# Performance work log

Hardware: AMD Instinct MI355X
Metric: run time of the kernel (lower is better)

The kernel has to match this reference:

```python
import jax, jax.numpy as jnp
import numpy as np

K = 20  # neighbors
SLOPE = 0.2  # leaky relu negative slope


def knn_idx(x):
    # x: [B, C, N] -> idx: [B, N, K] indices of K nearest points (incl. self)
    inner = -2.0 * jnp.einsum('bcn,bcm->bnm', x, x)          # [B,N,N]
    xx = jnp.sum(x * x, axis=1)                              # [B,N]
    pairwise = -xx[:, :, None] - inner - xx[:, None, :]      # negative sq dist
    _, idx = jax.lax.top_k(pairwise, K)                      # [B,N,K]
    return idx


def graph_feature(x, idx):
    # x: [B, C, N], idx: [B, N, K] -> [B, N, K, 2C] = cat(neighbor - center, center)
    xt = jnp.transpose(x, (0, 2, 1))                         # [B,N,C]
    nbr = jnp.take_along_axis(xt[:, None, :, :], idx[..., None], axis=2)  # [B,N,K,C]
    ctr = jnp.broadcast_to(xt[:, :, None, :], nbr.shape)     # [B,N,K,C]
    return jnp.concatenate([nbr - ctr, ctr], axis=-1)        # [B,N,K,2C]


def edge_block(x, W):
    # x: [B, C, N]; W: [C_out, 2C] (1x1 conv weight, no bias)
    f = graph_feature(x, knn_idx(x))                         # [B,N,K,2C]
    y = jnp.einsum('bnkc,oc->bonk', f, W)                    # [B,C_out,N,K]
    y = jax.nn.leaky_relu(y, negative_slope=SLOPE)
    return jnp.max(y, axis=-1)                               # [B,C_out,N]


def setup_inputs() -> dict:
    key = jax.random.key(0)
    ks = jax.random.split(key, 6)
    B, N = 8, 2048
    x = jax.random.normal(ks[0], (B, 3, N), dtype=jnp.float32)
    def w(k, o, i):
        return jax.random.normal(k, (o, i), dtype=jnp.float32) * (1.0 / np.sqrt(i))
    W1 = w(ks[1], 64, 6)      # block1: in 3  -> 64
    W2 = w(ks[2], 64, 128)    # block2: in 64 -> 64
    W3 = w(ks[3], 128, 128)   # block3: in 64 -> 128
    W4 = w(ks[4], 256, 256)   # block4: in 128-> 256
    Wg = w(ks[5], 1024, 512)  # global conv1d: 64+64+128+256=512 -> 1024
    return {'x': x, 'W1': W1, 'W2': W2, 'W3': W3, 'W4': W4, 'Wg': Wg}


def reference(x, W1, W2, W3, W4, Wg):
    x1 = edge_block(x, W1)                                   # [B,64,N]
    x2 = edge_block(x1, W2)                                  # [B,64,N]
    x3 = edge_block(x2, W3)                                  # [B,128,N]
    x4 = edge_block(x3, W4)                                  # [B,256,N]
    x_cat = jnp.concatenate([x1, x2, x3, x4], axis=1)        # [B,512,N]
    g = jnp.einsum('bcn,oc->bon', x_cat, Wg)                 # [B,1024,N]
    g = jax.nn.leaky_relu(g, negative_slope=SLOPE)
    return jnp.max(g, axis=-1)                               # [B,1024]
```

## Files before the change

kernel.cpp:

```cpp
#include <hip/hip_runtime.h>
#include <hip/hip_bf16.h>
#include <cfloat>

#define Nn 2048
#define KK 20
#define BB 8
#define SLOPE 0.2f
#define NCH 32

typedef __bf16 bf16x8 __attribute__((ext_vector_type(8)));
typedef float f32x4 __attribute__((ext_vector_type(4)));
typedef unsigned short u16x8 __attribute__((ext_vector_type(8)));

__device__ __forceinline__ unsigned short bfbits(__hip_bfloat16 h) {
    unsigned short us;
    __builtin_memcpy(&us, &h, 2);
    return us;
}


__global__ void wfrag_all(const float* __restrict__ W1, const float* __restrict__ W2,
                          const float* __restrict__ W3, const float* __restrict__ W4,
                          __hip_bfloat16* __restrict__ base) {
    int g = blockIdx.x * 256 + threadIdx.x;
    const float* W; int CIN, Co, CO2, KS; long hoff; int go;
    if (g < 512)        { go = g;        CIN = 3;   Co = 64;  CO2 = 128; KS = 1; hoff = 0;     W = W1; }
    else if (g < 1536)  { go = g - 512;  CIN = 64;  Co = 64;  CO2 = 128; KS = 2; hoff = 8192;  W = W2; }
    else if (g < 3584)  { go = g - 1536; CIN = 64;  Co = 128; CO2 = 256; KS = 2; hoff = 24576; W = W3; }
    else if (g < 11776) { go = g - 3584; CIN = 128; Co = 256; CO2 = 512; KS = 4; hoff = 57344; W = W4; }
    else return;
    int o = go / (KS * 4);
    int c8 = (go - o * (KS * 4)) * 8;
    long lsz = (long)(CO2 / 16) * KS * 512;
    __hip_bfloat16* Wh = base + hoff;
    __hip_bfloat16* Wl = Wh + lsz;
    u16x8 hw, lw;
    #pragma unroll
    for (int t = 0; t < 8; ++t) {
        int c = c8 + t;
        float v = 0.f;
        if (c < CIN) {
            if (o < Co) v = W[(long)o * 2 * CIN + c];
            else        v = W[(long)(o - Co) * 2 * CIN + CIN + c] - W[(long)(o - Co) * 2 * CIN + c];
        }
        __hip_bfloat16 h = __float2bfloat16(v);
        hw[t] = bfbits(h);
        lw[t] = bfbits(__float2bfloat16(v - __bfloat162float(h)));
    }
    long dst = ((long)(o >> 4) * KS + (c8 >> 5)) * 512 + ((o & 15) + 16 * ((c8 >> 3) & 3)) * 8;
    *(u16x8*)(Wh + dst) = hw;
    *(u16x8*)(Wl + dst) = lw;
}

__global__ void tobf16_frag(const float* __restrict__ W, __hip_bfloat16* __restrict__ F) {
    int g = blockIdx.x * 256 + threadIdx.x;
    if (g >= 1024 * 64) return;
    int o = g >> 6, k8 = (g & 63) * 8;
    const float* src = W + (long)o * 512 + k8;
    unsigned short tmp[8];
    #pragma unroll
    for (int t = 0; t < 8; ++t) tmp[t] = bfbits(__float2bfloat16(src[t]));
    long dst = ((long)(o >> 4) * 16 + (k8 >> 5)) * 512 + ((o & 15) + 16 * ((k8 >> 3) & 3)) * 8;
    u16x8 pk;
    #pragma unroll
    for (int t = 0; t < 8; ++t) pk[t] = tmp[t];
    *(u16x8*)(F + dst) = pk;
}

__global__ void split3_kernel(const float* __restrict__ x,
                              __hip_bfloat16* __restrict__ xh,
                              __hip_bfloat16* __restrict__ xl,
                              float* __restrict__ sq) {
    int i = blockIdx.x * 256 + threadIdx.x;
    if (i >= BB * Nn) return;
    const float* xb = x + (long)(i >> 11) * 3 * Nn + (i & 2047);
    float v0 = xb[0], v1 = xb[Nn], v2 = xb[2 * Nn];
    sq[i] = v0 * v0 + v1 * v1 + v2 * v2;
    __hip_bfloat16 h0 = __float2bfloat16(v0), h1 = __float2bfloat16(v1), h2 = __float2bfloat16(v2);
    __hip_bfloat16 l0 = __float2bfloat16(v0 - __bfloat162float(h0));
    __hip_bfloat16 l1 = __float2bfloat16(v1 - __bfloat162float(h1));
    __hip_bfloat16 l2 = __float2bfloat16(v2 - __bfloat162float(h2));
    long base = ((long)(i >> 11) * 128 + ((i & 2047) >> 4)) * 512 + (long)(i & 15) * 8;
    u16x8 z = (u16x8){0, 0, 0, 0, 0, 0, 0, 0};
    u16x8 hw = z, lw = z;
    hw[0] = bfbits(h0); hw[1] = bfbits(h1); hw[2] = bfbits(h2);
    lw[0] = bfbits(l0); lw[1] = bfbits(l1); lw[2] = bfbits(l2);
    *(u16x8*)(xh + base) = hw;
    *(u16x8*)(xl + base) = lw;
    #pragma unroll
    for (int q = 1; q < 4; ++q) {
        *(u16x8*)(xh + base + q * 128) = z;
        *(u16x8*)(xl + base + q * 128) = z;
    }
}

__device__ __forceinline__ unsigned fkey(float f) {
    unsigned u = __float_as_uint(f);
    return u ^ (((unsigned)((int)u >> 31)) | 0x80000000u);
}

template<int C, int NKS>
__global__ void __launch_bounds__(512)
gram_mfma(const __hip_bfloat16* __restrict__ xh, const __hip_bfloat16* __restrict__ xl,
          int ks0, const float* __restrict__ sqv, unsigned* __restrict__ Kbuf) {
    constexpr int KS = C / 32;
    const int tid = threadIdx.x;
    const int w = tid >> 6, lane = tid & 63;
    const int lm = lane & 15, quad = lane >> 4;
    const int wg = (blockIdx.x & 7) * 128 + (blockIdx.x >> 3);
    const int nb = wg & 7;
    const int mt = (wg >> 3) & 15;
    const int b  = wg >> 7;
    const int m0 = mt * 128 + (w >> 2) * 64;
    const int j0 = nb * 256 + (w & 3) * 64;

    const long TILE = (long)NKS * 512;
    const __hip_bfloat16* hbase = xh + (long)b * 128 * TILE + (long)ks0 * 512 + lane * 8;
    const __hip_bfloat16* lbase = xl + (long)b * 128 * TILE + (long)ks0 * 512 + lane * 8;
    const __hip_bfloat16* hA = hbase + (long)(m0 >> 4) * TILE;
    const __hip_bfloat16* lA = lbase + (long)(m0 >> 4) * TILE;
    const __hip_bfloat16* hB = hbase + (long)(j0 >> 4) * TILE;
    const __hip_bfloat16* lB = lbase + (long)(j0 >> 4) * TILE;

    f32x4 acc[4][4];
    #pragma unroll
    for (int i = 0; i < 4; ++i)
        #pragma unroll
        for (int j = 0; j < 4; ++j)
            acc[i][j] = (f32x4){0.f, 0.f, 0.f, 0.f};

    #pragma unroll 2
    for (int ks = 0; ks < KS; ++ks) {
        bf16x8 ah[4], alo[4], bh[4], blo[4];
        #pragma unroll
        for (int i = 0; i < 4; ++i) {
            ah[i]  = *(const bf16x8*)(const void*)(hA + (long)i * TILE + ks * 512);
            alo[i] = *(const bf16x8*)(const void*)(lA + (long)i * TILE + ks * 512);
        }
        #pragma unroll
        for (int j = 0; j < 4; ++j) {
            bh[j]  = *(const bf16x8*)(const void*)(hB + (long)j * TILE + ks * 512);
            blo[j] = *(const bf16x8*)(const void*)(lB + (long)j * TILE + ks * 512);
        }
        #pragma unroll
        for (int i = 0; i < 4; ++i)
            #pragma unroll
            for (int j = 0; j < 4; ++j) {
                acc[i][j] = __builtin_amdgcn_mfma_f32_16x16x32_bf16(alo[i], bh[j], acc[i][j], 0, 0, 0);
                acc[i][j] = __builtin_amdgcn_mfma_f32_16x16x32_bf16(ah[i], blo[j], acc[i][j], 0, 0, 0);
                acc[i][j] = __builtin_amdgcn_mfma_f32_16x16x32_bf16(ah[i], bh[j], acc[i][j], 0, 0, 0);
            }
    }

    const float* sqb = sqv + b * Nn;
    float sqj[4];
    #pragma unroll
    for (int j = 0; j < 4; ++j) sqj[j] = sqb[j0 + j * 16 + lm];

    unsigned* Kb = Kbuf + (long)b * Nn * Nn;
    #pragma unroll
    for (int i = 0; i < 4; ++i) {
        #pragma unroll
        for (int r = 0; r < 4; ++r) {
            int m = m0 + i * 16 + quad * 4 + r;
            uint4 kv;
            kv.x = fkey(fmaf(-2.f, acc[i][0][r], sqj[0]));
            kv.y = fkey(fmaf(-2.f, acc[i][1][r], sqj[1]));
            kv.z = fkey(fmaf(-2.f, acc[i][2][r], sqj[2]));
            kv.w = fkey(fmaf(-2.f, acc[i][3][r], sqj[3]));
            *(uint4*)(Kb + (long)m * Nn + j0 + lm * 4) = kv;
        }
    }
}

template<int KS, int NKS_A, int CO2>
__global__ void __launch_bounds__(256)
proj_mfma(const __hip_bfloat16* __restrict__ Ah, const __hip_bfloat16* __restrict__ Al,
          int ks0,
          const __hip_bfloat16* __restrict__ Wh, const __hip_bfloat16* __restrict__ Wl,
          float* __restrict__ Z) {
    constexpr int NWo = (CO2 >= 256) ? 4 : 2;
    constexpr int NWm = 4 / NWo;
    constexpr int MT = 2048 / (64 * NWm);
    const int tid = threadIdx.x;
    const int w = tid >> 6, lane = tid & 63;
    const int lm = lane & 15, quad = lane >> 4;
    const int b  = blockIdx.x & 7;
    const int mt = (blockIdx.x >> 3) % MT;
    const int ot = (blockIdx.x >> 3) / MT;
    const int m0 = mt * 64 * NWm + (w / NWo) * 64;
    const int o0 = ot * 64 * NWo + (w % NWo) * 64;

    const long TA = (long)NKS_A * 512;
    const long TW = (long)KS * 512;
    const __hip_bfloat16* hA = Ah + (long)b * 128 * TA + (long)(m0 >> 4) * TA + (long)ks0 * 512 + lane * 8;
    const __hip_bfloat16* lA = Al + (long)b * 128 * TA + (long)(m0 >> 4) * TA + (long)ks0 * 512 + lane * 8;
    const __hip_bfloat16* hW = Wh + (long)(o0 >> 4) * TW + lane * 8;
    const __hip_bfloat16* lW = Wl + (long)(o0 >> 4) * TW + lane * 8;

    f32x4 acc[4][4];
    #pragma unroll
    for (int i = 0; i < 4; ++i)
        #pragma unroll
        for (int j = 0; j < 4; ++j)
            acc[i][j] = (f32x4){0.f, 0.f, 0.f, 0.f};

    #pragma unroll 2
    for (int ks = 0; ks < KS; ++ks) {
        bf16x8 ah[4], alo[4], bh[4], blo[4];
        #pragma unroll
        for (int i = 0; i < 4; ++i) {
            ah[i]  = *(const bf16x8*)(const void*)(hA + (long)i * TA + ks * 512);
            alo[i] = *(const bf16x8*)(const void*)(lA + (long)i * TA + ks * 512);
        }
        #pragma unroll
        for (int j = 0; j < 4; ++j) {
            bh[j]  = *(const bf16x8*)(const void*)(hW + (long)j * TW + ks * 512);
            blo[j] = *(const bf16x8*)(const void*)(lW + (long)j * TW + ks * 512);
        }
        #pragma unroll
        for (int i = 0; i < 4; ++i)
            #pragma unroll
            for (int j = 0; j < 4; ++j) {
                acc[i][j] = __builtin_amdgcn_mfma_f32_16x16x32_bf16(alo[i], bh[j], acc[i][j], 0, 0, 0);
                acc[i][j] = __builtin_amdgcn_mfma_f32_16x16x32_bf16(ah[i], blo[j], acc[i][j], 0, 0, 0);
                acc[i][j] = __builtin_amdgcn_mfma_f32_16x16x32_bf16(ah[i], bh[j], acc[i][j], 0, 0, 0);
            }
    }

    float* Zb = Z + (long)b * 2048 * CO2;
    #pragma unroll
    for (int i = 0; i < 4; ++i) {
        #pragma unroll
        for (int r = 0; r < 4; ++r) {
            int n = m0 + i * 16 + quad * 4 + r;
            float* row = Zb + (long)n * CO2 + o0;
            #pragma unroll
            for (int j = 0; j < 4; ++j)
                row[j * 16 + lm] = acc[i][j][r];
        }
    }
}

__global__ void __launch_bounds__(512)
select_kernel(const unsigned* __restrict__ Kbuf, int* __restrict__ idx) {
    const int tid = threadIdx.x;
    const int b  = blockIdx.x >> 8;
    const int n0 = (blockIdx.x & 255) * 8;
    const int w = tid >> 6, lane = tid & 63;

    const unsigned* drow = Kbuf + ((long)b * Nn + n0 + w) * Nn;
    int* outp = idx + ((long)b * Nn + n0 + w) * KK;
    const int cbase = ((lane >> 4) << 6) + (lane & 15);

    unsigned mn = 0xFFFFFFFFu;
    #pragma unroll
    for (int jj = 0; jj < 8; ++jj) {
        int j4 = (jj * 64 + lane) * 4;
        uint4 v = *(const uint4*)(drow + j4);
        unsigned m01 = v.x < v.y ? v.x : v.y;
        unsigned m23 = v.z < v.w ? v.z : v.w;
        unsigned m = m01 < m23 ? m01 : m23;
        mn = m < mn ? m : mn;
    }

    unsigned T;
    {
        unsigned sa = mn;
        #pragma unroll
        for (int size = 2; size <= 64; size <<= 1) {
            #pragma unroll
            for (int str = size >> 1; str >= 1; str >>= 1) {
                const bool asc = ((lane & size) == 0);
                const bool keepmin = (((lane & str) == 0) == asc);
                unsigned pa = __shfl_xor(sa, str, 64);
                sa = keepmin ? (sa < pa ? sa : pa) : (sa > pa ? sa : pa);
            }
        }
        T = __shfl(sa, 19, 64);
    }

    unsigned long long c0 = 0, c1 = 0, c2 = 0, c3 = 0, c4 = 0, c5 = 0;
    unsigned cnt = 0;
    #pragma unroll
    for (int jj = 0; jj < 8; ++jj) {
        int j4 = (jj * 64 + lane) * 4;
        uint4 v = *(const uint4*)(drow + j4);
        int colb = jj * 256 + cbase;
        #pragma unroll
        for (int q = 0; q < 4; ++q) {
            unsigned kq = q == 0 ? v.x : q == 1 ? v.y : q == 2 ? v.z : v.w;
            if (kq <= T) {
                unsigned long long kv = ((unsigned long long)kq << 32) | (unsigned)(colb + q * 16);
                if (cnt == 0) c0 = kv;
                else if (cnt == 1) c1 = kv;
                else if (cnt == 2) c2 = kv;
                else if (cnt == 3) c3 = kv;
                else if (cnt == 4) c4 = kv;
                else if (cnt == 5) c5 = kv;
                ++cnt;
            }
        }
    }

    unsigned tot = cnt;
    #pragma unroll
    for (int s = 1; s < 64; s <<= 1) tot += __shfl_xor(tot, s, 64);
    unsigned long long anyovf = __ballot(cnt > 6);

    if (anyovf == 0 && tot <= 56) {
        int e = (int)tot - KK;
        for (int rr = 0; rr < e; ++rr) {
            unsigned long long mymax = c0;
            if (c1 > mymax) mymax = c1;
            if (c2 > mymax) mymax = c2;
            if (c3 > mymax) mymax = c3;
            if (c4 > mymax) mymax = c4;
            if (c5 > mymax) mymax = c5;
            unsigned long long wm = mymax;
            #pragma unroll
            for (int s = 1; s < 64; s <<= 1) {
                unsigned long long o = __shfl_xor(wm, s, 64);
                wm = o > wm ? o : wm;
            }
            if (mymax == wm) {
                if (c5 == wm) c5 = 0;
                else if (c4 == wm) c4 = 0;
                else if (c3 == wm) c3 = 0;
                else if (c2 == wm) c2 = 0;
                else if (c1 == wm) c1 = 0;
                else c0 = 0;
            }
        }
        unsigned myc = (c0 != 0) + (c1 != 0) + (c2 != 0) + (c3 != 0) + (c4 != 0) + (c5 != 0);
        unsigned inc = myc;
        #pragma unroll
        for (int off = 1; off < 64; off <<= 1) {
            unsigned t2 = __shfl_up(inc, off, 64);
            if (lane >= off) inc += t2;
        }
        int p = (int)(inc - myc);
        if (c0 != 0) outp[p++] = (int)(unsigned)c0;
        if (c1 != 0) outp[p++] = (int)(unsigned)c1;
        if (c2 != 0) outp[p++] = (int)(unsigned)c2;
        if (c3 != 0) outp[p++] = (int)(unsigned)c3;
        if (c4 != 0) outp[p++] = (int)(unsigned)c4;
        if (c5 != 0) outp[p++] = (int)(unsigned)c5;
        return;
    }

    unsigned exl[KK];
    int ne = 0;
    auto scan2x = [&](unsigned long long& m1, unsigned long long& m2) {
        m1 = ~0ull; m2 = ~0ull;
        for (int jj = 0; jj < 8; ++jj) {
            int j4 = (jj * 64 + lane) * 4;
            uint4 v = *(const uint4*)(drow + j4);
            int colb = jj * 256 + cbase;
            #pragma unroll
            for (int q = 0; q < 4; ++q) {
                unsigned kq = q == 0 ? v.x : q == 1 ? v.y : q == 2 ? v.z : v.w;
                unsigned col = (unsigned)(colb + q * 16);
                for (int t = 0; t < ne; ++t)
                    if (exl[t] == col) kq = 0xFFFFFFFFu;
                unsigned long long kv = ((unsigned long long)kq << 32) | col;
                unsigned long long hi = kv > m1 ? kv : m1;
                m1 = kv < m1 ? kv : m1;
                m2 = hi < m2 ? hi : m2;
            }
        }
    };

    unsigned long long lm1, lm2;
    scan2x(lm1, lm2);
    for (int k = 0; k < KK; ++k) {
        unsigned key = (unsigned)(lm1 >> 32);
        unsigned bk = key;
        #pragma unroll
        for (int s = 1; s < 64; s <<= 1) {
            unsigned ob = __shfl_xor(bk, s, 64);
            bk = ob < bk ? ob : bk;
        }
        unsigned long long winners = __ballot(key == bk);
        int wl = (int)(__ffsll((unsigned long long)winners) - 1);
        int bi = (int)__shfl((unsigned)lm1, wl, 64);
        if (lane == 0) outp[k] = bi;
        if (lane == wl) {
            exl[ne++] = (unsigned)bi;
            if (lm2 != ~0ull) { lm1 = lm2; lm2 = ~0ull; }
            else scan2x(lm1, lm2);
        }
    }
}

template<int CO, bool EMIT>
__global__ void __launch_bounds__(256)
gather_max(const float* __restrict__ Z, const int* __restrict__ idx,
           __hip_bfloat16* __restrict__ xbT, __hip_bfloat16* __restrict__ xbTlo,
           float* __restrict__ sqv, int coff) {
    constexpr int CO2 = 2 * CO;
    constexpr int VEC = CO / 64;
    __shared__ int ji[16][KK];
    const int tid = threadIdx.x;
    const int b  = blockIdx.x & 7;
    const int n0 = (blockIdx.x >> 3) * 16;
    const float* Zb = Z + (long)b * 2048 * CO2;

    for (int t = tid; t < 16 * KK; t += 256) {
        int nn = t / KK, k = t - nn * KK;
        ji[nn][k] = idx[((long)b * Nn + n0 + nn) * KK + k];
    }
    __syncthreads();

    const int w = tid >> 6, lane = tid & 63;
    for (int i = 0; i < 4; ++i) {
        int nl = w * 4 + i, n = n0 + nl;
        float mx[VEC];
        #pragma unroll
        for (int v = 0; v < VEC; ++v) mx[v] = -FLT_MAX;
        for (int k = 0; k < KK; ++k) {
            int m = ji[nl][k];
            const float* zr = Zb + (long)m * CO2 + lane * VEC;
            if constexpr (VEC == 4) {
                float4 zv = *(const float4*)zr;
                mx[0] = fmaxf(mx[0], zv.x); mx[1] = fmaxf(mx[1], zv.y);
                mx[2] = fmaxf(mx[2], zv.z); mx[3] = fmaxf(mx[3], zv.w);
            } else if constexpr (VEC == 2) {
                float2 zv = *(const float2*)zr;
                mx[0] = fmaxf(mx[0], zv.x); mx[1] = fmaxf(mx[1], zv.y);
            } else {
                mx[0] = fmaxf(mx[0], zr[0]);
            }
        }
        const float* zc = Zb + (long)n * CO2 + CO + lane * VEC;
        const int c0 = coff + lane * VEC;
        const long fbase = ((long)b * 128 + (n >> 4)) * 8192
                         + (long)(c0 >> 5) * 512
                         + (long)(((n & 15) + 16 * ((c0 >> 3) & 3)) * 8) + (c0 & 7);
        __hip_bfloat16* xr = xbT + fbase;
        float y[VEC];
        if constexpr (VEC == 4) {
            float4 cv = *(const float4*)zc;
            y[0] = mx[0] + cv.x; y[1] = mx[1] + cv.y; y[2] = mx[2] + cv.z; y[3] = mx[3] + cv.w;
        } else if constexpr (VEC == 2) {
            float2 cv = *(const float2*)zc;
            y[0] = mx[0] + cv.x; y[1] = mx[1] + cv.y;
        } else {
            y[0] = mx[0] + zc[0];
        }
        unsigned short hb[VEC], lb[VEC];
        float s = 0.f;
        #pragma unroll
        for (int v = 0; v < VEC; ++v) {
            y[v] = y[v] > 0.f ? y[v] : SLOPE * y[v];
            __hip_bfloat16 h = __float2bfloat16(y[v]);
            hb[v] = bfbits(h);
            if constexpr (EMIT) {
                lb[v] = bfbits(__float2bfloat16(y[v] - __bfloat162float(h)));
                s += y[v] * y[v];
            }
        }
        if constexpr (VEC == 4) {
            ushort4 pk; pk.x = hb[0]; pk.y = hb[1]; pk.z = hb[2]; pk.w = hb[3];
            *(ushort4*)xr = pk;
        } else if constexpr (VEC == 2) {
            ushort2 pk; pk.x = hb[0]; pk.y = hb[1];
            *(ushort2*)xr = pk;
        } else {
            *(unsigned short*)xr = hb[0];
        }
        if constexpr (EMIT) {
            __hip_bfloat16* lr = xbTlo + fbase;
            if constexpr (VEC == 4) {
                ushort4 pk; pk.x = lb[0]; pk.y = lb[1]; pk.z = lb[2]; pk.w = lb[3];
                *(ushort4*)lr = pk;
            } else if constexpr (VEC == 2) {
                ushort2 pk; pk.x = lb[0]; pk.y = lb[1];
                *(ushort2*)lr = pk;
            } else {
                *(unsigned short*)lr = lb[0];
            }
            #pragma unroll
            for (int off = 1; off < 64; off <<= 1) s += __shfl_xor(s, off, 64);
            if (lane == 0) sqv[b * Nn + n] = s;
        }
    }
}

__global__ void __launch_bounds__(512)
global_mfma(const __hip_bfloat16* __restrict__ Wgf,
            const __hip_bfloat16* __restrict__ xbT,
            float* __restrict__ partial) {
    const int tid = threadIdx.x;
    const int w = tid >> 6, lane = tid & 63;
    const int lm = lane & 15, quad = lane >> 4;
    const int wg = (blockIdx.x & 7) * 64 + (blockIdx.x >> 3);
    const int b  = wg >> 6;
    const int ot = (wg >> 3) & 7;
    const int nb = wg & 7;
    const int o0 = ot * 128 + (w >> 2) * 64;
    const int nbw = nb * 256 + (w & 3) * 64;

    const __hip_bfloat16* Af = Wgf + (long)(o0 >> 4) * 8192 + lane * 8;
    const __hip_bfloat16* Bf = xbT + ((long)b * 128 + (nbw >> 4)) * 8192 + lane * 8;

    f32x4 acc[4][4];
    #pragma unroll
    for (int mt = 0; mt < 4; ++mt)
        #pragma unroll
        for (int nt = 0; nt < 4; ++nt)
            acc[mt][nt] = (f32x4){0.f, 0.f, 0.f, 0.f};

    #pragma unroll 2
    for (int ks = 0; ks < 16; ++ks) {
        bf16x8 a[4], bb[4];
        #pragma unroll
        for (int mt = 0; mt < 4; ++mt)
            a[mt] = *(const bf16x8*)(const void*)(Af + (long)mt * 8192 + ks * 512);
        #pragma unroll
        for (int nt = 0; nt < 4; ++nt)
            bb[nt] = *(const bf16x8*)(const void*)(Bf + (long)nt * 8192 + ks * 512);
        #pragma unroll
        for (int mt = 0; mt < 4; ++mt)
            #pragma unroll
            for (int nt = 0; nt < 4; ++nt)
                acc[mt][nt] = __builtin_amdgcn_mfma_f32_16x16x32_bf16(
                    a[mt], bb[nt], acc[mt][nt], 0, 0, 0);
    }

    #pragma unroll
    for (int mt = 0; mt < 4; ++mt) {
        #pragma unroll
        for (int r = 0; r < 4; ++r) {
            float v = fmaxf(fmaxf(acc[mt][0][r], acc[mt][1][r]),
                            fmaxf(acc[mt][2][r], acc[mt][3][r]));
            #pragma unroll
            for (int s = 1; s < 16; s <<= 1)
                v = fmaxf(v, __shfl_xor(v, s, 16));
            if (lm == 0) {
                int o = o0 + mt * 16 + quad * 4 + r;
                partial[((long)b * 1024 + o) * NCH + nb * 4 + (w & 3)] = v;
            }
        }
    }
}

__global__ void gmax_kernel(const float* __restrict__ partial, float* __restrict__ out) {
    int i = blockIdx.x * 256 + threadIdx.x;
    float m = -FLT_MAX;
    #pragma unroll
    for (int j = 0; j < NCH; ++j) m = fmaxf(m, partial[(long)i * NCH + j]);
    out[i] = m > 0.f ? m : SLOPE * m;
}

extern "C" void kernel_launch(void* const* d_in, const int* in_sizes, int n_in,
                              void* d_out, int out_size, void* d_ws, size_t ws_size,
                              hipStream_t stream) {
    const float* x  = (const float*)d_in[0];
    const float* W1 = (const float*)d_in[1];
    const float* W2 = (const float*)d_in[2];
    const float* W3 = (const float*)d_in[3];
    const float* W4 = (const float*)d_in[4];
    const float* Wg = (const float*)d_in[5];
    float* out = (float*)d_out;

    int*   idxb = (int*)d_ws;
    float* part = (float*)(idxb + (long)BB * Nn * KK);
    __hip_bfloat16* Wgb = (__hip_bfloat16*)(part + (long)BB * 1024 * NCH);
    __hip_bfloat16* xbT = Wgb + (long)1024 * 512;
    __hip_bfloat16* xbTlo = xbT + (long)BB * Nn * 512;
    __hip_bfloat16* x1h = xbTlo + (long)BB * Nn * 512;
    __hip_bfloat16* x1l = x1h + (long)BB * Nn * 32;
    float* sq1  = (float*)(x1l + (long)BB * Nn * 32);
    float* sqv  = sq1 + (long)BB * Nn;
    __hip_bfloat16* wfb  = (__hip_bfloat16*)(sqv + (long)BB * Nn);
    __hip_bfloat16* wf1h = wfb;
    __hip_bfloat16* wf1l = wf1h + 8 * 512;
    __hip_bfloat16* wf2h = wf1l + 8 * 512;
    __hip_bfloat16* wf2l = wf2h + 8 * 2 * 512;
    __hip_bfloat16* wf3h = wf2l + 8 * 2 * 512;
    __hip_bfloat16* wf3l = wf3h + 16 * 2 * 512;
    __hip_bfloat16* wf4h = wf3l + 16 * 2 * 512;
    __hip_bfloat16* wf4l = wf4h + 32 * 4 * 512;
    float* Z    = (float*)(wf4l + 32 * 4 * 512);
    unsigned* Kbuf = (unsigned*)Z;

    wfrag_all<<<(11776 + 255) / 256, 256, 0, stream>>>(W1, W2, W3, W4, wfb);
    tobf16_frag<<<(1024 * 64 + 255) / 256, 256, 0, stream>>>(Wg, Wgb);
    split3_kernel<<<(BB * Nn) / 256, 256, 0, stream>>>(x, x1h, x1l, sq1);

    const int gram_grid = BB * 16 * 8;
    const int sel_grid  = BB * (Nn / 8);
    const int ep_grid   = (Nn / 16) * BB;

    gram_mfma<32, 1><<<gram_grid, 512, 0, stream>>>(x1h, x1l, 0, sq1, Kbuf);
    select_kernel<<<sel_grid, 512, 0, stream>>>(Kbuf, idxb);
    proj_mfma<1, 1, 128><<<8 * 16, 256, 0, stream>>>(x1h, x1l, 0, wf1h, wf1l, Z);
    gather_max<64, true><<<ep_grid, 256, 0, stream>>>(Z, idxb, xbT, xbTlo, sqv, 0);
    gram_mfma<64, 16><<<gram_grid, 512, 0, stream>>>(xbT, xbTlo, 0, sqv, Kbuf);
    select_kernel<<<sel_grid, 512, 0, stream>>>(Kbuf, idxb);
    proj_mfma<2, 16, 128><<<8 * 16, 256, 0, stream>>>(xbT, xbTlo, 0, wf2h, wf2l, Z);
    gather_max<64, true><<<ep_grid, 256, 0, stream>>>(Z, idxb, xbT, xbTlo, sqv, 64);
    gram_mfma<64, 16><<<gram_grid, 512, 0, stream>>>(xbT, xbTlo, 2, sqv, Kbuf);
    select_kernel<<<sel_grid, 512, 0, stream>>>(Kbuf, idxb);
    proj_mfma<2, 16, 256><<<8 * 32, 256, 0, stream>>>(xbT, xbTlo, 2, wf3h, wf3l, Z);
    gather_max<128, true><<<ep_grid, 256, 0, stream>>>(Z, idxb, xbT, xbTlo, sqv, 128);
    gram_mfma<128, 16><<<gram_grid, 512, 0, stream>>>(xbT, xbTlo, 4, sqv, Kbuf);
    select_kernel<<<sel_grid, 512, 0, stream>>>(Kbuf, idxb);
    proj_mfma<4, 16, 512><<<8 * 32 * 2, 256, 0, stream>>>(xbT, xbTlo, 4, wf4h, wf4l, Z);
    gather_max<256, false><<<ep_grid, 256, 0, stream>>>(Z, idxb, xbT, xbTlo, sqv, 256);

    global_mfma<<<BB * 8 * 8, 512, 0, stream>>>(Wgb, xbT, part);
    gmax_kernel<<<BB * 1024 / 256, 256, 0, stream>>>(part, out);
}
```

Before: 458.2 us.

## Fuse first-layer kNN distance and top-k selection into one register kernel

For the 3-channel first block, the MFMA Gram kernel plus the separate select pass are replaced by a single kernel. Each wavefront computes its point's exact squared distances in fp32 registers and finds a threshold from the per-lane minima with a bitonic sort. It keeps candidates under that threshold, trims them to 20, and falls back to iterative argmin when a lane has too many candidates. This avoids writing and re-reading the full 2048x2048 key buffer for layer one, but computes distances directly rather than through the Gram expansion, so tie ordering could differ from the reference.

```diff
diff --git a/kernel.cpp b/kernel.cpp
--- a/kernel.cpp
+++ b/kernel.cpp
@@ -99,6 +99,168 @@
     return u ^ (((unsigned)((int)u >> 31)) | 0x80000000u);
 }
 
+__global__ void __launch_bounds__(512)
+knn1_kernel(const float* __restrict__ x, int* __restrict__ idx) {
+    const int tid = threadIdx.x;
+    const int b  = blockIdx.x >> 8;
+    const int n0 = (blockIdx.x & 255) * 8;
+    const int w = tid >> 6, lane = tid & 63;
+    const int n = n0 + w;
+    const float* xb = x + (long)b * 3 * Nn;
+    int* outp = idx + ((long)b * Nn + n) * KK;
+
+    const float px = xb[n], py = xb[Nn + n], pz = xb[2 * Nn + n];
+
+    uint4 kk[8];
+    unsigned mn = 0xFFFFFFFFu;
+    #pragma unroll
+    for (int jj = 0; jj < 8; ++jj) {
+        int j4 = jj * 256 + lane * 4;
+        float4 qx = *(const float4*)(xb + j4);
+        float4 qy = *(const float4*)(xb + Nn + j4);
+        float4 qz = *(const float4*)(xb + 2 * Nn + j4);
+        float dx, dy, dz;
+        dx = qx.x - px; dy = qy.x - py; dz = qz.x - pz;
+        kk[jj].x = fkey(dx * dx + dy * dy + dz * dz);
+        dx = qx.y - px; dy = qy.y - py; dz = qz.y - pz;
+        kk[jj].y = fkey(dx * dx + dy * dy + dz * dz);
+        dx = qx.z - px; dy = qy.z - py; dz = qz.z - pz;
+        kk[jj].z = fkey(dx * dx + dy * dy + dz * dz);
+        dx = qx.w - px; dy = qy.w - py; dz = qz.w - pz;
+        kk[jj].w = fkey(dx * dx + dy * dy + dz * dz);
+        unsigned m01 = kk[jj].x < kk[jj].y ? kk[jj].x : kk[jj].y;
+        unsigned m23 = kk[jj].z < kk[jj].w ? kk[jj].z : kk[jj].w;
+        unsigned m = m01 < m23 ? m01 : m23;
+        mn = m < mn ? m : mn;
+    }
+
+    unsigned T;
+    {
+        unsigned sa = mn;
+        #pragma unroll
+        for (int size = 2; size <= 64; size <<= 1) {
+            #pragma unroll
+            for (int str = size >> 1; str >= 1; str >>= 1) {
+                const bool asc = ((lane & size) == 0);
+                const bool keepmin = (((lane & str) == 0) == asc);
+                unsigned pa = __shfl_xor(sa, str, 64);
+                sa = keepmin ? (sa < pa ? sa : pa) : (sa > pa ? sa : pa);
+            }
+        }
+        T = __shfl(sa, 19, 64);
+    }
+
+    unsigned long long c0 = 0, c1 = 0, c2 = 0, c3 = 0, c4 = 0, c5 = 0;
+    unsigned cnt = 0;
+    #pragma unroll
+    for (int jj = 0; jj < 8; ++jj) {
+        int j4 = jj * 256 + lane * 4;
+        uint4 v = kk[jj];
+        #pragma unroll
+        for (int q = 0; q < 4; ++q) {
+            unsigned kq = q == 0 ? v.x : q == 1 ? v.y : q == 2 ? v.z : v.w;
+            if (kq <= T) {
+                unsigned long long kv = ((unsigned long long)kq << 32) | (unsigned)(j4 + q);
+                if (cnt == 0) c0 = kv;
+                else if (cnt == 1) c1 = kv;
+                else if (cnt == 2) c2 = kv;
+                else if (cnt == 3) c3 = kv;
+                else if (cnt == 4) c4 = kv;
+                else if (cnt == 5) c5 = kv;
+                ++cnt;
+            }
+        }
+    }
+
+    unsigned tot = cnt;
+    #pragma unroll
+    for (int s = 1; s < 64; s <<= 1) tot += __shfl_xor(tot, s, 64);
+    unsigned long long anyovf = __ballot(cnt > 6);
+
+    if (anyovf == 0 && tot <= 56) {
+        int e = (int)tot - KK;
+        for (int rr = 0; rr < e; ++rr) {
+            unsigned long long mymax = c0;
+            if (c1 > mymax) mymax = c1;
+            if (c2 > mymax) mymax = c2;
+            if (c3 > mymax) mymax = c3;
+            if (c4 > mymax) mymax = c4;
+            if (c5 > mymax) mymax = c5;
+            unsigned long long wm = mymax;
+            #pragma unroll
+            for (int s = 1; s < 64; s <<= 1) {
+                unsigned long long o = __shfl_xor(wm, s, 64);
+                wm = o > wm ? o : wm;
+            }
+            if (mymax == wm) {
+                if (c5 == wm) c5 = 0;
+                else if (c4 == wm) c4 = 0;
+                else if (c3 == wm) c3 = 0;
+                else if (c2 == wm) c2 = 0;
+                else if (c1 == wm) c1 = 0;
+                else c0 = 0;
+            }
+        }
+        unsigned myc = (c0 != 0) + (c1 != 0) + (c2 != 0) + (c3 != 0) + (c4 != 0) + (c5 != 0);
+        unsigned inc = myc;
+        #pragma unroll
+        for (int off = 1; off < 64; off <<= 1) {
+            unsigned t2 = __shfl_up(inc, off, 64);
+            if (lane >= off) inc += t2;
+        }
+        int p = (int)(inc - myc);
+        if (c0 != 0) outp[p++] = (int)(unsigned)c0;
+        if (c1 != 0) outp[p++] = (int)(unsigned)c1;
+        if (c2 != 0) outp[p++] = (int)(unsigned)c2;
+        if (c3 != 0) outp[p++] = (int)(unsigned)c3;
+        if (c4 != 0) outp[p++] = (int)(unsigned)c4;
+        if (c5 != 0) outp[p++] = (int)(unsigned)c5;
+        return;
+    }
+
+    unsigned exl[KK];
+    int ne = 0;
+    auto scan2x = [&](unsigned long long& m1, unsigned long long& m2) {
+        m1 = ~0ull; m2 = ~0ull;
+        for (int jj = 0; jj < 8; ++jj) {
+            int j4 = jj * 256 + lane * 4;
+            uint4 v = kk[jj];
+            #pragma unroll
+            for (int q = 0; q < 4; ++q) {
+                unsigned kq = q == 0 ? v.x : q == 1 ? v.y : q == 2 ? v.z : v.w;
+                unsigned col = (unsigned)(j4 + q);
+                for (int t = 0; t < ne; ++t)
+                    if (exl[t] == col) kq = 0xFFFFFFFFu;
+                unsigned long long kv = ((unsigned long long)kq << 32) | col;
+                unsigned long long hi = kv > m1 ? kv : m1;
+                m1 = kv < m1 ? kv : m1;
+                m2 = hi < m2 ? hi : m2;
+            }
+        }
+    };
+
+    unsigned long long lm1, lm2;
+    scan2x(lm1, lm2);
+    for (int k = 0; k < KK; ++k) {
+        unsigned key = (unsigned)(lm1 >> 32);
+        unsigned bk = key;
+        #pragma unroll
+        for (int s = 1; s < 64; s <<= 1) {
+            unsigned ob = __shfl_xor(bk, s, 64);
+            bk = ob < bk ? ob : bk;
+        }
+        unsigned long long winners = __ballot(key == bk);
+        int wl = (int)(__ffsll((unsigned long long)winners) - 1);
+        int bi = (int)__shfl((unsigned)lm1, wl, 64);
+        if (lane == 0) outp[k] = bi;
+        if (lane == wl) {
+            exl[ne++] = (unsigned)bi;
+            if (lm2 != ~0ull) { lm1 = lm2; lm2 = ~0ull; }
+            else scan2x(lm1, lm2);
+        }
+    }
+}
+
 template<int C, int NKS>
 __global__ void __launch_bounds__(512)
 gram_mfma(const __hip_bfloat16* __restrict__ xh, const __hip_bfloat16* __restrict__ xl,
@@ -593,8 +755,7 @@
     const int sel_grid  = BB * (Nn / 8);
     const int ep_grid   = (Nn / 16) * BB;
 
-    gram_mfma<32, 1><<<gram_grid, 512, 0, stream>>>(x1h, x1l, 0, sq1, Kbuf);
-    select_kernel<<<sel_grid, 512, 0, stream>>>(Kbuf, idxb);
+    knn1_kernel<<<sel_grid, 512, 0, stream>>>(x, idxb);
     proj_mfma<1, 1, 128><<<8 * 16, 256, 0, stream>>>(x1h, x1l, 0, wf1h, wf1l, Z);
     gather_max<64, true><<<ep_grid, 256, 0, stream>>>(Z, idxb, xbT, xbTlo, sqv, 0);
     gram_mfma<64, 16><<<gram_grid, 512, 0, stream>>>(xbT, xbTlo, 0, sqv, Kbuf);
```

Measured after the change: 470.0 us. 2.6% more time.
